# Kernel optimization log

Hardware: AMD Instinct MI355X
Metric: run time of the kernel (lower is better)

Reference implementation:

```python
import jax, jax.numpy as jnp
import numpy as np

LEAK = 0.2

def leaky(x):
    return jnp.where(x > 0, x, LEAK * x)

def relu(x):
    return jnp.maximum(x, 0)

def conv1d(x, w):
    # x [B,Cin,L], w [Cout,Cin,3], stride 1, padding 1
    return jax.lax.conv_general_dilated(x, w, (1,), [(1, 1)],
        dimension_numbers=('NCH', 'OIH', 'NCH'))

def conv2d(x, w, pad, dil=1, groups=1):
    return jax.lax.conv_general_dilated(x, w, (1, 1), [(pad, pad), (pad, pad)],
        rhs_dilation=(dil, dil), feature_group_count=groups,
        dimension_numbers=('NCHW', 'OIHW', 'NCHW'))

def bn2d(x, p, eps=1e-5):
    # p: [4,C] = gamma, beta, running_mean, running_var (eval-mode BN)
    g, b, m, v = p
    s = (1, -1, 1, 1)
    return (x - m.reshape(s)) * (g.reshape(s) / jnp.sqrt(v.reshape(s) + eps)) + b.reshape(s)

def layernorm(x, g, b, eps=1e-5):
    mu = x.mean(-1, keepdims=True)
    var = ((x - mu) ** 2).mean(-1, keepdims=True)
    return (x - mu) / jnp.sqrt(var + eps) * g + b

def l2n(x, axis, eps):
    n = jnp.sqrt((x * x).sum(axis, keepdims=True))
    return x / jnp.maximum(n, eps)


def setup_inputs() -> dict:
    key = jax.random.key(0)
    B, C, H, W = 4, 64, 48, 48
    D, Fn, T, V = 256, 8, 4, 16
    E = 16  # orthogonal prototype embed dim
    ks = iter(jax.random.split(key, 64))
    def rn(shape, s=0.05):
        return jax.random.normal(next(ks), shape, jnp.float32) * s
    def bnp(c):
        return jnp.stack([1.0 + rn((c,), 0.1), rn((c,), 0.1), rn((c,), 0.1), 1.0 + jnp.abs(rn((c,), 0.1))])
    return dict(
        basis_vector_bank=jax.random.normal(next(ks), (T, V, D), jnp.float32),
        task_f=jax.random.normal(next(ks), (B, C, 16, 16), jnp.float32),
        img_f=jax.random.normal(next(ks), (B, C, H, W), jnp.float32),
        protos=jax.random.normal(next(ks), (T, E), jnp.float32),
        tA_w1=rn((E // 4, 1, 3)), tA_w2=rn((E // 2, E // 4, 3)),
        iA_w=rn((E // 2, C, 3, 3)), iA_bn=bnp(E // 2),
        at_w1=rn((E, Fn // 2 * E)), at_b1=rn((Fn // 2 * E,)),
        at_ln_g=jnp.ones((Fn // 2 * E,)), at_ln_b=jnp.zeros((Fn // 2 * E,)),
        at_w2=rn((Fn // 2 * E, Fn * E)), at_b2=rn((Fn * E,)),
        bv_t1=rn((D // 4, 1, 3)), bv_t2=rn((D // 2, D // 4, 3)),
        bv_ic1=rn((D // 4, C, 3, 3)), bv_bn1=bnp(D // 4),
        bv_ic2=rn((D // 2, D // 4, 3, 3)), bv_bn2=bnp(D // 2),
        bv_w1=rn((D, D // 4)), bv_b1=rn((D // 4,)),
        bv_ln_g=jnp.ones((D // 4,)), bv_ln_b=jnp.zeros((D // 4,)),
        bv_w2=rn((D // 4, D)), bv_b2=rn((D,)),
        m1_w1=rn((D, D // 4)), m1_b1=rn((D // 4,)),
        m1_ln_g=jnp.ones((D // 4,)), m1_ln_b=jnp.zeros((D // 4,)),
        m1_w2=rn((D // 4, C * C)), m1_b2=rn((C * C,)),
        m3_w1=rn((D, D // 4)), m3_b1=rn((D // 4,)),
        m3_ln_g=jnp.ones((D // 4,)), m3_ln_b=jnp.zeros((D // 4,)),
        m3_w2=rn((D // 4, 9 * C * C)), m3_b2=rn((9 * C * C,)),
        blr_bn=bnp(C),
        zc_w=rn((C, C, 1, 1), 0.01), zc_b=rn((C,), 0.01),
    )


def _forward(basis_vector_bank, task_f, img_f, protos, tA_w1, tA_w2, iA_w, iA_bn,
             at_w1, at_b1, at_ln_g, at_ln_b, at_w2, at_b2,
             bv_t1, bv_t2, bv_ic1, bv_bn1, bv_ic2, bv_bn2,
             bv_w1, bv_b1, bv_ln_g, bv_ln_b, bv_w2, bv_b2,
             m1_w1, m1_b1, m1_ln_g, m1_ln_b, m1_w2, m1_b2,
             m3_w1, m3_b1, m3_ln_g, m3_ln_b, m3_w2, m3_b2,
             blr_bn, zc_w, zc_b):
    T, V, D = basis_vector_bank.shape
    B, C, H, W = img_f.shape
    E = protos.shape[1]
    Fn = at_w2.shape[1] // E
    tau = 0.5

    # --- A2SI routing features ---
    xt = task_f.reshape(B, 1, -1)
    t1 = conv1d(leaky(conv1d(xt, tA_w1)), tA_w2).mean(-1)          # [B,E/2]
    i1 = leaky(bn2d(conv2d(img_f, iA_w, 1), iA_bn)).mean((2, 3))   # [B,E/2]
    f1 = jnp.concatenate([t1, i1], axis=1)                         # [B,E]
    h = relu(layernorm(f1 @ at_w1 + at_b1, at_ln_g, at_ln_b))
    tif = (h @ at_w2 + at_b2).reshape(B, E, Fn)                    # [B,E,F]
    logits = jnp.einsum('te,bef->bft', l2n(protos, -1, 1e-8), l2n(tif, 1, 1e-8))  # [B,F,T]

    # hard gumbel-softmax (straight-through), fixed noise key for determinism
    u = jax.random.uniform(jax.random.key(42), logits.shape, jnp.float32, 1e-10, 1.0)
    g = -jnp.log(-jnp.log(u))
    y = jax.nn.softmax((logits + g) / tau, axis=-1)
    idx = jnp.argmax(y, axis=-1)                                   # [B,F]
    y_hard = jax.nn.one_hot(idx, T, dtype=y.dtype)
    set_type = y_hard + y - jax.lax.stop_gradient(y)

    bank_flat = basis_vector_bank.reshape(T, V * D)
    sbvb = jnp.einsum('bft,tk->bfk', set_type, bank_flat).reshape(B, Fn, V, D)

    # --- BasisV_filter: filter feature ---
    xt2 = task_f.reshape(B, C, -1)
    rms = jnp.sqrt((xt2 ** 2).mean((1, 2), keepdims=True))
    xt2 = (xt2 / (rms + 1e-8)).reshape(B, 1, -1)
    te = conv1d(leaky(conv1d(xt2, bv_t1)), bv_t2).mean(-1)         # [B,D/2]
    ie = leaky(bn2d(conv2d(img_f, bv_ic1, 1), bv_bn1))
    ie = leaky(bn2d(conv2d(ie, bv_ic2, 1), bv_bn2)).mean((2, 3))   # [B,D/2]
    ff = jnp.concatenate([te, ie], axis=1)                         # [B,D]
    ff = relu(layernorm(ff @ bv_w1 + bv_b1, bv_ln_g, bv_ln_b)) @ bv_w2 + bv_b2

    # --- per-(batch,type) group gather/top-k/scatter, vectorized ---
    # group bank = bank of first filter with that type (hard one-hot -> type's bank)
    occ = idx[:, None, :] == jnp.arange(T)[None, :, None]          # [B,T,F]
    first = jnp.argmax(occ, axis=-1)                               # [B,T]
    Bg = jnp.take_along_axis(sbvb, first[:, :, None, None], axis=1)  # [B,T,V,D]
    # all rows of Q within a group are identical (filter_f expanded over F),
    # so S.max(0) == cosine(ff[b], Bg[b,t])
    scores = jnp.einsum('bd,btvd->btv', l2n(ff, -1, 1e-12), l2n(Bg, -1, 1e-12))
    order = jnp.argsort(-scores, axis=-1)                          # [B,T,V] topk order
    lt = jnp.tril(jnp.ones((Fn, Fn), bool), -1)                    # j < i
    rank = ((idx[:, :, None] == idx[:, None, :]) & lt).sum(-1)     # position in group
    bidx = jnp.arange(B)[:, None]
    sel = order[bidx, idx, rank]                                   # [B,F]
    bvf = Bg[bidx, idx, sel]                                       # [B,F,D]

    # --- per-filter dynamic convolutions ---
    w1 = relu(layernorm(bvf @ m1_w1 + m1_b1, m1_ln_g, m1_ln_b)) @ m1_w2 + m1_b2
    w1 = w1.reshape(B, Fn, C, C)                                   # [B,F,out,in]
    w3 = relu(layernorm(bvf @ m3_w1 + m3_b1, m3_ln_g, m3_ln_b)) @ m3_w2 + m3_b2
    w3 = w3.reshape(B * Fn, C, C, 3, 3)

    dp0 = jnp.einsum('bfoc,bchw->bfohw', w1, img_f)                # 1x1 branch
    xin = jnp.broadcast_to(img_f[:, None], (B, Fn, C, H, W)).reshape(1, B * Fn * C, H, W)
    ker = w3.reshape(B * Fn * C, C, 3, 3)
    dpd = [conv2d(xin, ker, d, dil=d, groups=B * Fn).reshape(B, Fn, C, H, W)
           for d in (1, 2, 3)]                                     # same-padded dilated 3x3
    t_ = idx[:, :, None, None, None]
    dp = jnp.where(t_ == 0, dp0, jnp.where(t_ == 1, dpd[0],
         jnp.where(t_ == 2, dpd[1], dpd[2])))                      # [B,F,C,H,W]

    x = leaky(bn2d(dp.reshape(B * Fn, C, H, W), blr_bn)).reshape(B, Fn, C, H, W).mean(1)
    a = conv2d(x, zc_w, 0) + zc_b.reshape(1, -1, 1, 1)
    return a + img_f


@jax.jit
def reference(basis_vector_bank, task_f, img_f, protos, tA_w1, tA_w2, iA_w, iA_bn,
              at_w1, at_b1, at_ln_g, at_ln_b, at_w2, at_b2,
              bv_t1, bv_t2, bv_ic1, bv_bn1, bv_ic2, bv_bn2,
              bv_w1, bv_b1, bv_ln_g, bv_ln_b, bv_w2, bv_b2,
              m1_w1, m1_b1, m1_ln_g, m1_ln_b, m1_w2, m1_b2,
              m3_w1, m3_b1, m3_ln_g, m3_ln_b, m3_w2, m3_b2,
              blr_bn, zc_w, zc_b):
    return _forward(basis_vector_bank, task_f, img_f, protos, tA_w1, tA_w2, iA_w, iA_bn,
                    at_w1, at_b1, at_ln_g, at_ln_b, at_w2, at_b2,
                    bv_t1, bv_t2, bv_ic1, bv_bn1, bv_ic2, bv_bn2,
                    bv_w1, bv_b1, bv_ln_g, bv_ln_b, bv_w2, bv_b2,
                    m1_w1, m1_b1, m1_ln_g, m1_ln_b, m1_w2, m1_b2,
                    m3_w1, m3_b1, m3_ln_g, m3_ln_b, m3_w2, m3_b2,
                    blr_bn, zc_w, zc_b)
```

## Files before the change

kernel.cpp:

```cpp
#include <hip/hip_runtime.h>
#include <math.h>

#define LEAKC 0.2f

#define NB 4
#define NC 64
#define LLEN 16384
#define HW 2304
#define PP 54
#define PHW 2916
#define SLABP 72
#define CP 72
#define IE1C 50

typedef __attribute__((ext_vector_type(8))) short short8;
typedef __attribute__((ext_vector_type(4))) float floatx4;

__device__ __forceinline__ float leaky(float x){ return x > 0.f ? x : LEAKC*x; }

__device__ __forceinline__ float wave_sum64(float v){
  for(int off=32;off;off>>=1) v += __shfl_xor(v,off);
  return v;
}

__device__ __forceinline__ unsigned short f2bf(float x){
  unsigned u=__float_as_uint(x);
  unsigned r=u+0x7FFFu+((u>>16)&1u);
  return (unsigned short)(r>>16);
}

__device__ __forceinline__ void threefry2x32(unsigned k0, unsigned k1, unsigned& x0, unsigned& x1){
  unsigned ks0=k0, ks1=k1, ks2=k0^k1^0x1BD11BDAu;
  x0+=ks0; x1+=ks1;
  const int rot0[4]={13,15,26,6};
  const int rot1[4]={17,29,16,24};
#define TF_APPLY(rr) {for(int r=0;r<4;r++){x0+=x1; x1=(x1<<rr[r])|(x1>>(32-rr[r])); x1^=x0;}}
  TF_APPLY(rot0); x0+=ks1; x1+=ks2+1u;
  TF_APPLY(rot1); x0+=ks2; x1+=ks0+2u;
  TF_APPLY(rot0); x0+=ks0; x1+=ks1+3u;
  TF_APPLY(rot1); x0+=ks1; x1+=ks2+4u;
  TF_APPLY(rot0); x0+=ks2; x1+=ks0+5u;
#undef TF_APPLY
}

__device__ __forceinline__ float jax_uniform128(int i){
  unsigned x0=0u, x1=(unsigned)i;
  threefry2x32(0u,42u,x0,x1);
  unsigned bits = x0 ^ x1;
  unsigned fb=(bits>>9)|0x3f800000u;
  float f=__uint_as_float(fb)-1.0f;
  float u=f*(1.0f-1e-10f)+1e-10f;
  return fmaxf(1e-10f,u);
}

struct MidSM {
  float sT[64], s0[64], sL[64];
  float red8[64][9];
  float totA_s[4]; float rms_s;
  float part[512];
  float te_s[128], t1_s[8];
  float f1[16], h[64], tif[128], tifn[128], tden[8], pden[4], pn[64], z[32];
  int sidx[8], sfirst[4], srank[8], rows[8];
  float iered[128];
  float fbuf[256], hh[64], ffn_s[256], finv_s;
  float scores[64];
  int order[64];
  float bvf[2048];
};

__global__ __launch_bounds__(256) void k_pre(const float* __restrict__ task_f,
                      const float* __restrict__ w1A, const float* __restrict__ w1B,
                      float* __restrict__ totApart, float* __restrict__ a0A, float* __restrict__ aLA,
                      float* __restrict__ totBpart, float* __restrict__ a0B, float* __restrict__ aLB,
                      float* __restrict__ rmspart,
                      const float* __restrict__ img,
                      const float* __restrict__ w1, const float* __restrict__ w2,
                      const float* __restrict__ wa,
                      unsigned short* __restrict__ imgTP,
                      unsigned short* __restrict__ W1T, unsigned short* __restrict__ W2T,
                      unsigned short* __restrict__ WAT,
                      const float* __restrict__ mw1, const float* __restrict__ mw3,
                      const float* __restrict__ bvw1p, const float* __restrict__ bvw2p,
                      const float* __restrict__ bvt2p, const float* __restrict__ atw2p,
                      const float* __restrict__ bankp,
                      const float* __restrict__ m1w2p, const float* __restrict__ m3w2p,
                      const float* __restrict__ zcwp,
                      float* __restrict__ warm, int* __restrict__ donec){
  if(blockIdx.x<256){
    int b=blockIdx.x>>6, seg=blockIdx.x&63;
    const float* x=task_f+b*LLEN;
    float tA[4]={0,0,0,0};
    float tB[64];
#pragma unroll
    for(int c=0;c<64;c++) tB[c]=0.f;
    float sq=0.f;
    int l=seg*256+threadIdx.x;
    {
      float xm=(l>0)?x[l-1]:0.f;
      float xc=x[l];
      float xp=(l<LLEN-1)?x[l+1]:0.f;
      sq=xc*xc;
#pragma unroll
      for(int c=0;c<4;c++){
        float a=leaky(w1A[c*3+0]*xm + w1A[c*3+1]*xc + w1A[c*3+2]*xp);
        tA[c]=a;
        if(l==0) a0A[b*4+c]=a;
        if(l==LLEN-1) aLA[b*4+c]=a;
      }
#pragma unroll
      for(int c=0;c<64;c++){
        float a=leaky(w1B[c*3+0]*xm + w1B[c*3+1]*xc + w1B[c*3+2]*xp);
        tB[c]=a;
        if(l==0) a0B[b*64+c]=a;
        if(l==LLEN-1) aLB[b*64+c]=a;
      }
    }
    sq=wave_sum64(sq);
#pragma unroll
    for(int c=0;c<4;c++) tA[c]=wave_sum64(tA[c]);
#pragma unroll
    for(int c=0;c<64;c++){
      float v=tB[c];
      for(int off=32;off;off>>=1) v+=__shfl_down(v,off);
      tB[c]=v;
    }
    __shared__ float redB[4][64];
    __shared__ float redA[4][4];
    __shared__ float redQ[4];
    int wave=threadIdx.x>>6, lane=threadIdx.x&63;
    if(lane==0){
#pragma unroll
      for(int c=0;c<64;c++) redB[wave][c]=tB[c];
#pragma unroll
      for(int c=0;c<4;c++) redA[wave][c]=tA[c];
      redQ[wave]=sq;
    }
    __syncthreads();
    if(threadIdx.x<64){
      float s=redB[0][threadIdx.x]+redB[1][threadIdx.x]+redB[2][threadIdx.x]+redB[3][threadIdx.x];
      totBpart[(size_t)(b*64+seg)*64+threadIdx.x]=s;
    } else if(threadIdx.x<68){
      int c=threadIdx.x-64;
      totApart[(b*64+seg)*4+c]=redA[0][c]+redA[1][c]+redA[2][c]+redA[3][c];
    } else if(threadIdx.x==68){
      rmspart[b*64+seg]=redQ[0]+redQ[1]+redQ[2]+redQ[3];
    }
  } else if(blockIdx.x<400){
    int blk=blockIdx.x-256;
    int b=blk/36, t=blk%36;
    int p0=t*64;
    __shared__ float tile[64][65];
    int pp=threadIdx.x&63, c4=threadIdx.x>>6;
    for(int r=0;r<16;r++){
      int c=c4*16+r;
      tile[c][pp]=img[(b*64+c)*HW + p0+pp];
    }
    __syncthreads();
    int pxl=threadIdx.x>>2, cg=(threadIdx.x&3)*16;
    unsigned out[8];
#pragma unroll
    for(int q=0;q<8;q++){
      unsigned lo=f2bf(tile[cg+2*q][pxl]);
      unsigned hi=f2bf(tile[cg+2*q+1][pxl]);
      out[q]=lo|(hi<<16);
    }
    int px=p0+pxl;
    int h=px/48, w=px-h*48;
    int poff=(h+3)*PP+(w+3);
    unsigned* dst=(unsigned*)(imgTP + ((size_t)(b*PHW+poff))*64 + cg);
#pragma unroll
    for(int q=0;q<8;q++) dst[q]=out[q];
  } else if(blockIdx.x<868){
    int n=(blockIdx.x-400)*256+threadIdx.x;
    if(n<9*64*64){
      int tap=n>>12, oc=(n>>6)&63, c=n&63;
      W1T[n]=f2bf(w1[oc*576+c*9+tap]);
    } else if(n<9*64*64+9*128*64){
      int m=n-9*64*64;
      int tap=m/8192, r=m-tap*8192, oc=r>>6, c=r&63;
      W2T[m]=f2bf(w2[oc*576+c*9+tap]);
    } else {
      int q=n-9*64*64-9*128*64;
      if(q<9*16*64){
        int tap=q>>10, r=q&1023, o=r>>6, c=r&63;
        WAT[q]=(o<8)?f2bf(wa[o*576+c*9+tap]):(unsigned short)0;
      }
    }
  } else if(blockIdx.x<932){
    int t=(blockIdx.x-868)*256+threadIdx.x;
    float a=0.f;
    for(int i=t;i*16<16384;i+=16384) a+=mw1[i*16];
    for(int i=t;i*16<16384;i+=16384) a+=mw3[i*16];
    for(int i=t;i*16<16384;i+=16384) a+=bvw1p[i*16];
    for(int i=t;i*16<16384;i+=16384) a+=bvw2p[i*16];
    for(int i=t;i*16<24576;i+=16384) a+=bvt2p[i*16];
    for(int i=t;i*16<8192;i+=16384) a+=atw2p[i*16];
    for(int i=t;i*16<16384;i+=16384) a+=bankp[i*16];
    for(int i=t;i*16<262144;i+=16384) a+=m1w2p[i*16];
    for(int i=t;i*16<2359296;i+=16384) a+=m3w2p[i*16];
    for(int i=t;i*16<4096;i+=16384) a+=zcwp[i*16];
    warm[t&1023]=a;
  } else {
    if(blockIdx.x==932 && threadIdx.x==0) *donec=0;
    int id=(blockIdx.x-932)*256+threadIdx.x;
    uint4 z=make_uint4(0,0,0,0);
    for(int cch=id;cch<19584;cch+=4096){
      int ck=cch&7, pxid=cch>>3;
      int b=pxid/612, p=pxid-b*612;
      int h,w;
      if(p<324){ int r=p/54; w=p-r*54; h=(r<3)?r:(r+48); }
      else { int q=p-324; int r2=q/6; int cc=q-r2*6; h=3+r2; w=(cc<3)?cc:(cc+48); }
      *(uint4*)(imgTP + ((size_t)(b*PHW + h*PP + w))*64 + ck*8)=z;
    }
  }
}

__global__ __launch_bounds__(512) void k_cm(const unsigned short* __restrict__ imgTP,
    const unsigned short* __restrict__ W1T, const unsigned short* __restrict__ W2T,
    const unsigned short* __restrict__ WAT,
    const float* __restrict__ bn1, const float* __restrict__ bn2, const float* __restrict__ bnA,
    float* __restrict__ iepart, float* __restrict__ i1part,
    const float* __restrict__ totApart, const float* __restrict__ a0A, const float* __restrict__ aLA,
    const float* __restrict__ totBpart, const float* __restrict__ a0B, const float* __restrict__ aLB,
    const float* __restrict__ rmspart,
    const float* __restrict__ tA_w2, const float* __restrict__ bv_t2,
    const float* __restrict__ at_w1, const float* __restrict__ at_b1,
    const float* __restrict__ at_ln_g, const float* __restrict__ at_ln_b,
    const float* __restrict__ at_w2, const float* __restrict__ at_b2,
    const float* __restrict__ protos,
    const float* __restrict__ bv_w1, const float* __restrict__ bv_b1,
    const float* __restrict__ bv_ln_g, const float* __restrict__ bv_ln_b,
    const float* __restrict__ bv_w2, const float* __restrict__ bv_b2,
    const float* __restrict__ bank,
    const float* __restrict__ m1_w1, const float* __restrict__ m1_b1,
    const float* __restrict__ m1_g,  const float* __restrict__ m1_bb,
    const float* __restrict__ m3_w1, const float* __restrict__ m3_b1,
    const float* __restrict__ m3_g,  const float* __restrict__ m3_bb,
    int* __restrict__ idxo, float* __restrict__ hid1, float* __restrict__ hid3,
    int* __restrict__ donec){
  __shared__ __align__(16) char smraw[75456];
  int tid=threadIdx.x;
  int lane=tid&63, wv=tid>>6;
  int n0=lane&15, kg=lane>>4;
  if(blockIdx.x<96){
    int blk=blockIdx.x;
    int b=blk/24, hp=blk-b*24;
    int h0=hp*2;
    unsigned short* slab=(unsigned short*)smraw;
    unsigned short* ie1=(unsigned short*)(smraw+46656);
    {
      const unsigned short* ibase=imgTP+((size_t)b*PHW+(size_t)(h0+1)*PP)*64;
      for(int e=tid;e<6*54*8;e+=512){
        int rr=e/(54*8), rem=e-rr*54*8, w=rem>>3, ck=rem&7;
        uint4 v=*(const uint4*)(ibase+((size_t)(rr*PP+w))*64+ck*8);
        *(uint4*)(slab+(rr*54+w)*SLABP+ck*8)=v;
      }
      if(tid<64){
        int br=tid>>4, cq=(tid>>3)&1, ck=tid&7;
        *(uint4*)(ie1+((size_t)(br*IE1C+(cq?49:0)))*CP+ck*8)=make_uint4(0,0,0,0);
      }
    }
    __syncthreads();
    {
      int mt=wv&3, rh=wv>>2;
      floatx4 acc[2][3];
#pragma unroll
      for(int rr=0;rr<2;rr++)
#pragma unroll
        for(int nt=0;nt<3;nt++) acc[rr][nt]=(floatx4){0.f,0.f,0.f,0.f};
#pragma unroll
      for(int ti=0;ti<3;ti++){
#pragma unroll
        for(int tj=0;tj<3;tj++){
          int tap=ti*3+tj;
          const unsigned short* Ab=W1T+(size_t)tap*4096;
#pragma unroll
          for(int c0=0;c0<64;c0+=32){
            short8 a=*(const short8*)(Ab+((mt*16+n0)*64+c0+kg*8));
#pragma unroll
            for(int rr=0;rr<2;rr++){
              int sr=rh*2+rr+ti;
#pragma unroll
              for(int nt=0;nt<3;nt++){
                int sc=nt*16+n0+tj+2;
                short8 bv=*(const short8*)(slab+(sr*54+sc)*SLABP+c0+kg*8);
                acc[rr][nt]=__builtin_amdgcn_mfma_f32_16x16x32_bf16(a,bv,acc[rr][nt],0,0,0);
              }
            }
          }
        }
      }
      int obase=mt*16+kg*4;
      float scale[4],m_[4],be_[4];
#pragma unroll
      for(int reg=0;reg<4;reg++){
        int o=obase+reg;
        scale[reg]=bn1[o]/sqrtf(bn1[192+o]+1e-5f);
        m_[reg]=bn1[128+o]; be_[reg]=bn1[64+o];
      }
#pragma unroll
      for(int rr=0;rr<2;rr++){
        int br=rh*2+rr;
        bool rv=((unsigned)(h0-1+br))<48u;
#pragma unroll
        for(int nt=0;nt<3;nt++){
          float v0=rv?leaky((acc[rr][nt][0]-m_[0])*scale[0]+be_[0]):0.f;
          float v1=rv?leaky((acc[rr][nt][1]-m_[1])*scale[1]+be_[1]):0.f;
          float v2=rv?leaky((acc[rr][nt][2]-m_[2])*scale[2]+be_[2]):0.f;
          float v3=rv?leaky((acc[rr][nt][3]-m_[3])*scale[3]+be_[3]):0.f;
          unsigned w0=f2bf(v0)|((unsigned)f2bf(v1)<<16);
          unsigned w1=f2bf(v2)|((unsigned)f2bf(v3)<<16);
          uint2 pk={w0,w1};
          *(uint2*)(ie1+((size_t)(br*IE1C+(nt*16+1+n0)))*CP+obase)=pk;
        }
      }
    }
    __syncthreads();
    {
      int mt2=wv;
      floatx4 acc[6];
#pragma unroll
      for(int i=0;i<6;i++) acc[i]=(floatx4){0.f,0.f,0.f,0.f};
#pragma unroll
      for(int ti=0;ti<3;ti++){
#pragma unroll
        for(int tj=0;tj<3;tj++){
          int tap=ti*3+tj;
          const unsigned short* Ab=W2T+(size_t)tap*8192;
#pragma unroll
          for(int c0=0;c0<64;c0+=32){
            short8 a=*(const short8*)(Ab+((mt2*16+n0)*64+c0+kg*8));
#pragma unroll
            for(int rr=0;rr<2;rr++){
              int sr=rr+ti;
#pragma unroll
              for(int wc=0;wc<3;wc++){
                int q=wc*16+n0+tj;
                short8 bv=*(const short8*)(ie1+((size_t)(sr*IE1C+q))*CP+c0+kg*8);
                acc[rr*3+wc]=__builtin_amdgcn_mfma_f32_16x16x32_bf16(a,bv,acc[rr*3+wc],0,0,0);
              }
            }
          }
        }
      }
      int obase=mt2*16+kg*4;
#pragma unroll
      for(int reg=0;reg<4;reg++){
        int o=obase+reg;
        float scale=bn2[o]/sqrtf(bn2[384+o]+1e-5f);
        float m_=bn2[256+o], be_=bn2[128+o];
        float part=0;
#pragma unroll
        for(int i=0;i<6;i++) part+=leaky((acc[i][reg]-m_)*scale+be_);
        for(int off=1;off<16;off<<=1) part+=__shfl_xor(part,off);
        if(n0==0) iepart[(b*24+hp)*128+o]=part*(1.f/2304.f);
      }
    }
    __syncthreads();
    if(tid==0) __hip_atomic_fetch_add(donec,1,__ATOMIC_RELEASE,__HIP_MEMORY_SCOPE_AGENT);
  } else if(blockIdx.x<108){
    int blk2=blockIdx.x-96;
    int b=blk2/3, hg=blk2%3;
    int hp=hg*8+wv;
    int h0=hp*2;
    const unsigned short* ib=imgTP+(size_t)b*PHW*64;
    floatx4 acc[6];
#pragma unroll
    for(int i=0;i<6;i++) acc[i]=(floatx4){0.f,0.f,0.f,0.f};
#pragma unroll
    for(int ti=0;ti<3;ti++){
#pragma unroll
      for(int tj=0;tj<3;tj++){
        int tap=ti*3+tj;
        const unsigned short* Ab=WAT+(size_t)tap*1024;
#pragma unroll
        for(int c0=0;c0<64;c0+=32){
          short8 a=*(const short8*)(Ab+(n0*64+c0+kg*8));
#pragma unroll
          for(int rr=0;rr<2;rr++){
            int r=h0+rr+ti-1+3;
#pragma unroll
            for(int wc=0;wc<3;wc++){
              int w=wc*16+n0+tj-1+3;
              short8 bv=*(const short8*)(ib+((size_t)(r*PP+w)*64+c0+kg*8));
              acc[rr*3+wc]=__builtin_amdgcn_mfma_f32_16x16x32_bf16(a,bv,acc[rr*3+wc],0,0,0);
            }
          }
        }
      }
    }
    int obase=kg*4;
#pragma unroll
    for(int reg=0;reg<4;reg++){
      int o=obase+reg;
      float part=0;
      if(o<8){
        float scale=bnA[o]/sqrtf(bnA[24+o]+1e-5f);
        float m_=bnA[16+o], be_=bnA[8+o];
#pragma unroll
        for(int i=0;i<6;i++) part+=leaky((acc[i][reg]-m_)*scale+be_);
      }
      for(int off=1;off<16;off<<=1) part+=__shfl_xor(part,off);
      if(n0==0 && o<8) i1part[(b*24+hp)*8+o]=part*(1.f/2304.f);
    }
    __syncthreads();
    if(tid==0) __hip_atomic_fetch_add(donec,1,__ATOMIC_RELEASE,__HIP_MEMORY_SCOPE_AGENT);
  } else {
    MidSM* S=(MidSM*)smraw;
    int b=blockIdx.x-108;
    const float invL=1.0f/16384.0f;
    {
      int c8=tid>>3, g8=tid&7;
      float s8=0;
#pragma unroll
      for(int seg=g8*8;seg<g8*8+8;seg++) s8+=totBpart[(size_t)(b*64+seg)*64+c8];
      S->red8[c8][g8]=s8;
    }
    if(tid>=64 && tid<128){
      int t=tid-64;
      S->s0[t]=a0B[b*64+t]; S->sL[t]=aLB[b*64+t];
    } else if(tid>=128 && tid<192){
      float v=rmspart[b*64+(tid-128)];
      v=wave_sum64(v);
      if(tid==128) S->rms_s=v;
    } else if(tid>=192 && tid<196){
      int c=tid-192;
      float s=0;
#pragma unroll 8
      for(int seg=0;seg<64;seg++) s+=totApart[(b*64+seg)*4+c];
      S->totA_s[c]=s;
    }
    __syncthreads();
    if(tid<64){
      float s=0;
#pragma unroll
      for(int g=0;g<8;g++) s+=S->red8[tid][g];
      S->sT[tid]=s;
    }
    __syncthreads();
    float scB=1.0f/(sqrtf(S->rms_s*invL)+1e-8f);
    if(tid<256){
      int c2=tid&127, h2=tid>>7;
      const float* wr=bv_t2+c2*192;
      float s=0;
      for(int c1=h2*32;c1<h2*32+32;c1+=8){
        float4 q[6];
        const float4* r4=(const float4*)(wr+c1*3);
#pragma unroll
        for(int u=0;u<6;u++) q[u]=r4[u];
        const float* qq=(const float*)q;
#pragma unroll
        for(int u=0;u<8;u++){
          int c=c1+u;
          float T=S->sT[c], A0=S->s0[c], AL=S->sL[c];
          s += qq[u*3+0]*(T-AL) + qq[u*3+1]*T + qq[u*3+2]*(T-A0);
        }
      }
      S->part[tid]=s;
    } else if(tid>=384 && tid<392){
      int c2=tid-384;
      float s=0;
      for(int c1=0;c1<4;c1++){
        float T=S->totA_s[c1], A0=a0A[b*4+c1], AL=aLA[b*4+c1];
        const float* w=&tA_w2[(c2*4+c1)*3];
        s += w[0]*(T-AL) + w[1]*T + w[2]*(T-A0);
      }
      S->t1_s[c2]=s*invL;
    }
    __syncthreads();
    if(tid<128) S->te_s[tid]=(S->part[tid]+S->part[tid+128])*invL*scB;
    __syncthreads();
    if(tid==0){
      while(__hip_atomic_load(donec,__ATOMIC_ACQUIRE,__HIP_MEMORY_SCOPE_AGENT)<108)
        __builtin_amdgcn_s_sleep(8);
    }
    __syncthreads();
    if(tid<8) S->f1[tid]=S->t1_s[tid];
    else if(tid<16){
      int f=tid-8;
      float s=0;
#pragma unroll
      for(int g=0;g<24;g++) s+=i1part[(b*24+g)*8+f];
      S->f1[tid]=s;
    } else if(tid>=256 && tid<384){
      int c=tid-256;
      float s=0;
#pragma unroll 8
      for(int g=0;g<24;g++) s+=iepart[(b*24+g)*128+c];
      S->iered[c]=s;
    }
    __syncthreads();
    if(tid<64){
      float s=at_b1[lane];
#pragma unroll
      for(int i=0;i<16;i++) s+=S->f1[i]*at_w1[i*64+lane];
      float mu=wave_sum64(s)*(1.f/64.f);
      float d=s-mu;
      float var=wave_sum64(d*d)*(1.f/64.f);
      S->h[lane]=fmaxf(d*(1.0f/sqrtf(var+1e-5f))*at_ln_g[lane]+at_ln_b[lane],0.f);
    }
    __syncthreads();
    if(tid<256){
      int n=tid&127, h2=tid>>7;
      float a0=0,a1=0;
      for(int k=h2*32;k<h2*32+32;k+=2){
        a0+=S->h[k]*at_w2[k*128+n];
        a1+=S->h[k+1]*at_w2[(k+1)*128+n];
      }
      S->part[tid]=a0+a1;
    }
    __syncthreads();
    if(tid<128) S->tif[tid]=at_b2[tid]+S->part[tid]+S->part[tid+128];
    __syncthreads();
    if(tid<8){
      int f=tid;
      float ss=0; for(int e=0;e<16;e++){float v=S->tif[e*8+f]; ss+=v*v;}
      S->tden[f]=fmaxf(sqrtf(ss),1e-8f);
    } else if(tid<12){
      int t=tid-8;
      float ss=0; for(int e=0;e<16;e++){float v=protos[t*16+e]; ss+=v*v;}
      S->pden[t]=fmaxf(sqrtf(ss),1e-8f);
    }
    __syncthreads();
    if(tid<128) S->tifn[tid]=S->tif[tid]/S->tden[tid&7];
    if(tid<64) S->pn[tid]=protos[tid]/S->pden[tid>>4];
    __syncthreads();
    if(tid<32){
      int f=tid>>2, t=tid&3;
      float ss=0;
#pragma unroll
      for(int e=0;e<16;e++) ss+=S->pn[t*16+e]*S->tifn[e*8+f];
      float u=jax_uniform128(b*32+f*4+t);
      float g=-logf(-logf(u));
      S->z[tid]=ss+g;
    }
    __syncthreads();
    if(tid<8){
      float best=S->z[tid*4]; int bi=0;
      for(int t=1;t<4;t++){ float v=S->z[tid*4+t]; if(v>best){best=v;bi=t;} }
      S->sidx[tid]=bi;
    }
    __syncthreads();
    if(tid<4){
      int t=tid;
      int fi=0;
      for(int f=7;f>=0;f--) if(S->sidx[f]==t) fi=f;
      S->sfirst[t]=fi;
    } else if(tid<12){
      int f=tid-4;
      int c=0; for(int f2=0;f2<f;f2++) if(S->sidx[f2]==S->sidx[f]) c++;
      S->srank[f]=c;
    }
    __syncthreads();

    if(tid<128) S->fbuf[tid]=S->te_s[tid];
    else if(tid<256) S->fbuf[tid]=S->iered[tid-128];
    __syncthreads();
    if(tid<256){
      int l64=tid&63, q=tid>>6;
      float a0=0,a1=0,a2=0,a3=0;
      for(int k=q*64;k<q*64+64;k+=4){
        a0+=S->fbuf[k]  *bv_w1[k*64+l64];
        a1+=S->fbuf[k+1]*bv_w1[(k+1)*64+l64];
        a2+=S->fbuf[k+2]*bv_w1[(k+2)*64+l64];
        a3+=S->fbuf[k+3]*bv_w1[(k+3)*64+l64];
      }
      S->part[tid]=((a0+a1)+(a2+a3));
    }
    __syncthreads();
    if(tid<64){
      float s=bv_b1[lane]+S->part[lane]+S->part[64+lane]+S->part[128+lane]+S->part[192+lane];
      float mu=wave_sum64(s)*(1.f/64.f);
      float d=s-mu;
      float var=wave_sum64(d*d)*(1.f/64.f);
      S->hh[lane]=fmaxf(d*(1.0f/sqrtf(var+1e-5f))*bv_ln_g[lane]+bv_ln_b[lane],0.f);
    }
    __syncthreads();
    {
      int n=tid&255, h2=tid>>8;
      float a0=0,a1=0;
      for(int k=h2*32;k<h2*32+32;k+=2){
        a0+=S->hh[k]*bv_w2[k*256+n];
        a1+=S->hh[k+1]*bv_w2[(k+1)*256+n];
      }
      S->part[tid]=a0+a1;
    }
    __syncthreads();
    if(tid<256) S->ffn_s[tid]=bv_b2[tid]+S->part[tid]+S->part[tid+256];
    __syncthreads();
    if(tid<64){
      float sq=0;
#pragma unroll
      for(int u=0;u<4;u++){ float v=S->ffn_s[u*64+lane]; sq+=v*v; }
      sq=wave_sum64(sq);
      if(lane==0) S->finv_s=1.0f/fmaxf(sqrtf(sq),1e-12f);
    }
    __syncthreads();
    if(tid<256) S->ffn_s[tid]*=S->finv_s;
    __syncthreads();

    if(tid<128){
      int it=tid&63, h2=tid>>6;
      int t=it>>4, v=it&15;
      int tt=S->sidx[S->sfirst[t]];
      const float4* row=(const float4*)(bank+(tt*16+v)*256);
      float sa=0,na=0;
      for(int d4=h2*32;d4<h2*32+32;d4++){
        float4 r=row[d4];
        const float* fp=&S->ffn_s[d4*4];
        sa+=fp[0]*r.x+fp[1]*r.y+fp[2]*r.z+fp[3]*r.w;
        na+=r.x*r.x+r.y*r.y+r.z*r.z+r.w*r.w;
      }
      S->part[tid]=sa;
      S->part[256+tid]=na;
    }
    __syncthreads();
    if(tid<64) S->scores[tid]=(S->part[tid]+S->part[tid+64])/fmaxf(sqrtf(S->part[256+tid]+S->part[320+tid]),1e-12f);
    __syncthreads();
    if(tid<4){
      const float* sc=&S->scores[tid*16];
      unsigned used=0;
      for(int pk=0;pk<16;pk++){
        int best=-1; float bv=-1e30f;
        for(int v2=0;v2<16;v2++){
          if(used&(1u<<v2)) continue;
          float vv=sc[v2];
          if(best<0||vv>bv){bv=vv;best=v2;}
        }
        used|=1u<<best;
        S->order[tid*16+pk]=best;
      }
    }
    __syncthreads();
    if(tid<8){
      int t=S->sidx[tid];
      int v=S->order[t*16+S->srank[tid]];
      S->rows[tid]=t*16+v;
      idxo[b*8+tid]=t;
    }
    __syncthreads();

    for(int ii=tid;ii<2048;ii+=512){
      int r=ii>>8, d=ii&255;
      S->bvf[ii]=bank[S->rows[r]*256+d];
    }
    __syncthreads();
    {
      int r=wv;
      const float* bp=&S->bvf[r*256];
      float a0=0,a1=0,a2=0,a3=0;
      float c0=0,c1=0,c2=0,c3=0;
      for(int d=0;d<256;d+=4){
        float b0=bp[d],b1=bp[d+1],b2=bp[d+2],b3=bp[d+3];
        a0+=b0*m1_w1[d*64+lane];
        a1+=b1*m1_w1[(d+1)*64+lane];
        a2+=b2*m1_w1[(d+2)*64+lane];
        a3+=b3*m1_w1[(d+3)*64+lane];
        c0+=b0*m3_w1[d*64+lane];
        c1+=b1*m3_w1[(d+1)*64+lane];
        c2+=b2*m3_w1[(d+2)*64+lane];
        c3+=b3*m3_w1[(d+3)*64+lane];
      }
      float s1=m1_b1[lane]+((a0+a1)+(a2+a3));
      float s3=m3_b1[lane]+((c0+c1)+(c2+c3));
      float mu=wave_sum64(s1)*(1.f/64.f);
      float dd=s1-mu;
      float var=wave_sum64(dd*dd)*(1.f/64.f);
      hid1[(b*8+r)*64+lane]=fmaxf(dd*(1.0f/sqrtf(var+1e-5f))*m1_g[lane]+m1_bb[lane],0.f);
      mu=wave_sum64(s3)*(1.f/64.f);
      dd=s3-mu;
      var=wave_sum64(dd*dd)*(1.f/64.f);
      hid3[(b*8+r)*64+lane]=fmaxf(dd*(1.0f/sqrtf(var+1e-5f))*m3_g[lane]+m3_bb[lane],0.f);
    }
  }
}

__global__ __launch_bounds__(256) void k_heads(const float* __restrict__ hid1, const float* __restrict__ hid3,
                        const float* __restrict__ w2a, const float* __restrict__ b2a,
                        const float* __restrict__ w2b, const float* __restrict__ b2b,
                        unsigned short* __restrict__ A1, unsigned short* __restrict__ A3){
  __shared__ float hl[2048];
  if(blockIdx.x<16){
    int n=blockIdx.x*256+threadIdx.x;
    float wcol[64];
#pragma unroll
    for(int k=0;k<64;k++) wcol[k]=w2a[k*4096+n];
    float bb=b2a[n];
    for(int i=threadIdx.x;i<2048;i+=256) hl[i]=hid1[i];
    __syncthreads();
    for(int bf=0;bf<32;bf++){
      float s=bb;
#pragma unroll
      for(int k=0;k<64;k++) s+=hl[bf*64+k]*wcol[k];
      A1[bf*4096+n]=f2bf(s);
    }
  } else {
    int n=(blockIdx.x-16)*256+threadIdx.x;
    float wcol[64];
#pragma unroll
    for(int k=0;k<64;k++) wcol[k]=w2b[(size_t)k*36864+n];
    float bb=b2b[n];
    for(int i=threadIdx.x;i<2048;i+=256) hl[i]=hid3[i];
    __syncthreads();
    int o=n/576, rem=n-o*576;
    int c=rem/9, tap=rem-c*9;
    size_t base=((size_t)tap*64+o)*64+c;
    for(int bf=0;bf<32;bf++){
      float s=bb;
#pragma unroll
      for(int k=0;k<64;k++) s+=hl[bf*64+k]*wcol[k];
      A3[(size_t)bf*9*4096+base]=f2bf(s);
    }
  }
}

__global__ __launch_bounds__(512) void k_dynF(const unsigned short* __restrict__ imgTP,
                       const unsigned short* __restrict__ A1, const unsigned short* __restrict__ A3,
                       const int* __restrict__ idx, const float* __restrict__ bn,
                       const float* __restrict__ zc_w, const float* __restrict__ zc_b,
                       const float* __restrict__ img, float* __restrict__ out){
  int blk=blockIdx.x;
  int b=blk/48, r0=blk-b*48;
  int tid=threadIdx.x;
  int lane=tid&63, w8=tid>>6;
  int mt=w8&3, fh=w8>>2;
  int n0=lane&15, kg=lane>>4;
  __shared__ unsigned short slab[7*54*SLABP];
  __shared__ float xl[64*50];
  __shared__ float zl[4096];
  int tts[4];
#pragma unroll
  for(int i=0;i<4;i++) tts[i]=idx[b*8+fh*4+i];
  int obase=mt*16+kg*4;
  float scale[4],m_[4],be_[4];
#pragma unroll
  for(int reg=0;reg<4;reg++){
    int o=obase+reg;
    scale[reg]=bn[o]/sqrtf(bn[192+o]+1e-5f);
    m_[reg]=bn[128+o]; be_[reg]=bn[64+o];
  }
  for(int i=tid;i<4096;i+=512) zl[i]=zc_w[i];
  for(int i=tid;i<3200;i+=512) xl[i]=0.f;
  {
    const unsigned short* ibase=imgTP+((size_t)b*PHW+(size_t)r0*PP)*64;
    for(int e=tid;e<7*54*8;e+=512){
      int rr=e/(54*8), rem=e-rr*54*8, w=rem>>3, ck=rem&7;
      uint4 v=*(const uint4*)(ibase + ((size_t)(rr*PP+w))*64 + ck*8);
      *(uint4*)(slab + (rr*54+w)*SLABP + ck*8)=v;
    }
  }
  __syncthreads();
  float xsum[3][4];
#pragma unroll
  for(int wc=0;wc<3;wc++)
#pragma unroll
    for(int reg=0;reg<4;reg++) xsum[wc][reg]=0.f;
#pragma unroll
  for(int fi=0;fi<4;fi++){
    int f=fh*4+fi;
    int bf=b*8+f;
    int tt=tts[fi];
    floatx4 acc[3];
#pragma unroll
    for(int i=0;i<3;i++) acc[i]=(floatx4){0.f,0.f,0.f,0.f};
    if(tt==0){
      const unsigned short* Ab=A1+(size_t)bf*4096;
#pragma unroll
      for(int c0=0;c0<64;c0+=32){
        short8 a=*(const short8*)(Ab+((mt*16+n0)*64+c0+kg*8));
#pragma unroll
        for(int wc=0;wc<3;wc++){
          short8 bv=*(const short8*)(slab + (3*54 + wc*16+n0+3)*SLABP + c0+kg*8);
          acc[wc]=__builtin_amdgcn_mfma_f32_16x16x32_bf16(a,bv,acc[wc],0,0,0);
        }
      }
    } else {
      int d=tt;
      const unsigned short* A3b=A3+(size_t)bf*9*4096;
#pragma unroll
      for(int ti=0;ti<3;ti++){
        int lr=d*(ti-1)+3;
#pragma unroll
        for(int tj=0;tj<3;tj++){
          int tap=ti*3+tj;
          int dw=d*(tj-1)+3;
          const unsigned short* Ab=A3b+(size_t)tap*4096;
#pragma unroll
          for(int c0=0;c0<64;c0+=32){
            short8 a=*(const short8*)(Ab+((mt*16+n0)*64+c0+kg*8));
#pragma unroll
            for(int wc=0;wc<3;wc++){
              short8 bv=*(const short8*)(slab + (lr*54 + wc*16+n0+dw)*SLABP + c0+kg*8);
              acc[wc]=__builtin_amdgcn_mfma_f32_16x16x32_bf16(a,bv,acc[wc],0,0,0);
            }
          }
        }
      }
    }
#pragma unroll
    for(int wc=0;wc<3;wc++)
#pragma unroll
      for(int reg=0;reg<4;reg++)
        xsum[wc][reg]+=leaky((acc[wc][reg]-m_[reg])*scale[reg]+be_[reg]);
  }
#pragma unroll
  for(int wc=0;wc<3;wc++)
#pragma unroll
    for(int reg=0;reg<4;reg++)
      atomicAdd(&xl[(obase+reg)*50 + wc*16+n0], xsum[wc][reg]*0.125f);
  __syncthreads();
  size_t base=(size_t)b*64*HW + r0*48;
  for(int e=tid;e<3072;e+=512){
    int o=e/48, px=e-o*48;
    float s=zc_b[o];
#pragma unroll
    for(int c=0;c<64;c++) s+=zl[o*64+c]*xl[c*50+px];
    size_t a=base+(size_t)o*HW+px;
    out[a]=s+img[a];
  }
}

extern "C" void kernel_launch(void* const* d_in, const int* in_sizes, int n_in,
                              void* d_out, int out_size, void* d_ws, size_t ws_size,
                              hipStream_t stream){
  const float* bank   =(const float*)d_in[0];
  const float* task_f =(const float*)d_in[1];
  const float* img_f  =(const float*)d_in[2];
  const float* protos =(const float*)d_in[3];
  const float* tA_w1  =(const float*)d_in[4];
  const float* tA_w2  =(const float*)d_in[5];
  const float* iA_w   =(const float*)d_in[6];
  const float* iA_bn  =(const float*)d_in[7];
  const float* at_w1  =(const float*)d_in[8];
  const float* at_b1  =(const float*)d_in[9];
  const float* at_ln_g=(const float*)d_in[10];
  const float* at_ln_b=(const float*)d_in[11];
  const float* at_w2  =(const float*)d_in[12];
  const float* at_b2  =(const float*)d_in[13];
  const float* bv_t1  =(const float*)d_in[14];
  const float* bv_t2  =(const float*)d_in[15];
  const float* bv_ic1 =(const float*)d_in[16];
  const float* bv_bn1 =(const float*)d_in[17];
  const float* bv_ic2 =(const float*)d_in[18];
  const float* bv_bn2 =(const float*)d_in[19];
  const float* bv_w1  =(const float*)d_in[20];
  const float* bv_b1  =(const float*)d_in[21];
  const float* bv_ln_g=(const float*)d_in[22];
  const float* bv_ln_b=(const float*)d_in[23];
  const float* bv_w2  =(const float*)d_in[24];
  const float* bv_b2  =(const float*)d_in[25];
  const float* m1_w1  =(const float*)d_in[26];
  const float* m1_b1  =(const float*)d_in[27];
  const float* m1_ln_g=(const float*)d_in[28];
  const float* m1_ln_b=(const float*)d_in[29];
  const float* m1_w2  =(const float*)d_in[30];
  const float* m1_b2  =(const float*)d_in[31];
  const float* m3_w1  =(const float*)d_in[32];
  const float* m3_b1  =(const float*)d_in[33];
  const float* m3_ln_g=(const float*)d_in[34];
  const float* m3_ln_b=(const float*)d_in[35];
  const float* m3_w2  =(const float*)d_in[36];
  const float* m3_b2  =(const float*)d_in[37];
  const float* blr_bn =(const float*)d_in[38];
  const float* zc_w   =(const float*)d_in[39];
  const float* zc_b   =(const float*)d_in[40];

  float* ws=(float*)d_ws;
  float* totApart=ws+0;
  float* a0A  =ws+1024;
  float* aLA  =ws+1040;
  float* totBpart=ws+1056;
  float* a0B  =ws+17440;
  float* aLB  =ws+17696;
  float* rmspart=ws+17952;
  float* i1part =ws+18208;
  float* iepart =ws+18976;
  int*   idxp   =(int*)(ws+31264);
  float* hid1=ws+31296;
  float* hid3=ws+33344;
  unsigned short* A1p  =(unsigned short*)(ws+35392);
  unsigned short* A3p  =(unsigned short*)(ws+100928);
  unsigned short* imgTP=(unsigned short*)(ws+690752);
  unsigned short* W1Tp =(unsigned short*)(ws+1064000);
  unsigned short* W2Tp =(unsigned short*)(ws+1082432);
  unsigned short* WATp =(unsigned short*)(ws+1119296);
  float* warm =ws+1123904;
  int*   donec=(int*)(ws+1124928);

  k_pre<<<948,256,0,stream>>>(task_f, tA_w1, bv_t1,
                              totApart, a0A, aLA, totBpart, a0B, aLB, rmspart,
                              img_f, bv_ic1, bv_ic2, iA_w, imgTP, W1Tp, W2Tp, WATp,
                              m1_w1, m3_w1, bv_w1, bv_w2, bv_t2, at_w2, bank,
                              m1_w2, m3_w2, zc_w, warm, donec);
  k_cm<<<112,512,0,stream>>>(imgTP, W1Tp, W2Tp, WATp, bv_bn1, bv_bn2, iA_bn,
                             iepart, i1part,
                             totApart, a0A, aLA, totBpart, a0B, aLB, rmspart,
                             tA_w2, bv_t2,
                             at_w1, at_b1, at_ln_g, at_ln_b, at_w2, at_b2, protos,
                             bv_w1, bv_b1, bv_ln_g, bv_ln_b, bv_w2, bv_b2, bank,
                             m1_w1, m1_b1, m1_ln_g, m1_ln_b,
                             m3_w1, m3_b1, m3_ln_g, m3_ln_b,
                             idxp, hid1, hid3, donec);
  k_heads<<<160,256,0,stream>>>(hid1, hid3, m1_w2, m1_b2, m3_w2, m3_b2, A1p, A3p);
  k_dynF<<<192,512,0,stream>>>(imgTP, A1p, A3p, idxp, blr_bn, zc_w, zc_b, img_f, (float*)d_out);

  (void)in_sizes; (void)n_in; (void)out_size; (void)ws_size;
}
```

Measured before the change: 266.1 us.

## Fuse head GEMV kernel into k_cm with per-stage atomic counters

Removes the separate k_heads launch by adding 80 extra blocks to k_cm that prefetch their weight columns into registers and then spin-wait on a counter set by the four mid blocks before computing A1/A3. The single done counter is split into per-stage counters, so the mid blocks wait only on the 12 i1 blocks first and defer the wait on the 96 conv blocks until the iepart reduction is actually needed. This overlaps weight loading and mid-stage work with the conv blocks and removes one launch boundary. The cost is extra spinning blocks, and correctness depends on all 192 blocks being co-resident to avoid deadlock.

```diff
diff --git a/kernel.cpp b/kernel.cpp
--- a/kernel.cpp
+++ b/kernel.cpp
@@ -61,7 +61,6 @@
   float te_s[128], t1_s[8];
   float f1[16], h[64], tif[128], tifn[128], tden[8], pden[4], pn[64], z[32];
   int sidx[8], sfirst[4], srank[8], rows[8];
-  float iered[128];
   float fbuf[256], hh[64], ffn_s[256], finv_s;
   float scores[64];
   int order[64];
@@ -85,7 +84,7 @@
                       const float* __restrict__ bankp,
                       const float* __restrict__ m1w2p, const float* __restrict__ m3w2p,
                       const float* __restrict__ zcwp,
-                      float* __restrict__ warm, int* __restrict__ donec){
+                      float* __restrict__ warm, int* __restrict__ cnt){
   if(blockIdx.x<256){
     int b=blockIdx.x>>6, seg=blockIdx.x&63;
     const float* x=task_f+b*LLEN;
@@ -201,7 +200,8 @@
     for(int i=t;i*16<4096;i+=16384) a+=zcwp[i*16];
     warm[t&1023]=a;
   } else {
-    if(blockIdx.x==932 && threadIdx.x==0) *donec=0;
+    if(blockIdx.x==932 && threadIdx.x<4)
+      __hip_atomic_store(&cnt[threadIdx.x],0,__ATOMIC_RELAXED,__HIP_MEMORY_SCOPE_AGENT);
     int id=(blockIdx.x-932)*256+threadIdx.x;
     uint4 z=make_uint4(0,0,0,0);
     for(int cch=id;cch<19584;cch+=4096){
@@ -236,8 +236,11 @@
     const float* __restrict__ m1_g,  const float* __restrict__ m1_bb,
     const float* __restrict__ m3_w1, const float* __restrict__ m3_b1,
     const float* __restrict__ m3_g,  const float* __restrict__ m3_bb,
+    const float* __restrict__ m1_w2, const float* __restrict__ m1_b2,
+    const float* __restrict__ m3_w2, const float* __restrict__ m3_b2,
+    unsigned short* __restrict__ A1, unsigned short* __restrict__ A3,
     int* __restrict__ idxo, float* __restrict__ hid1, float* __restrict__ hid3,
-    int* __restrict__ donec){
+    int* __restrict__ cnt){
   __shared__ __align__(16) char smraw[75456];
   int tid=threadIdx.x;
   int lane=tid&63, wv=tid>>6;
@@ -357,7 +360,7 @@
       }
     }
     __syncthreads();
-    if(tid==0) __hip_atomic_fetch_add(donec,1,__ATOMIC_RELEASE,__HIP_MEMORY_SCOPE_AGENT);
+    if(tid==0) __hip_atomic_fetch_add(&cnt[0],1,__ATOMIC_RELEASE,__HIP_MEMORY_SCOPE_AGENT);
   } else if(blockIdx.x<108){
     int blk2=blockIdx.x-96;
     int b=blk2/3, hg=blk2%3;
@@ -404,8 +407,8 @@
       if(n0==0 && o<8) i1part[(b*24+hp)*8+o]=part*(1.f/2304.f);
     }
     __syncthreads();
-    if(tid==0) __hip_atomic_fetch_add(donec,1,__ATOMIC_RELEASE,__HIP_MEMORY_SCOPE_AGENT);
-  } else {
+    if(tid==0) __hip_atomic_fetch_add(&cnt[1],1,__ATOMIC_RELEASE,__HIP_MEMORY_SCOPE_AGENT);
+  } else if(blockIdx.x<112){
     MidSM* S=(MidSM*)smraw;
     int b=blockIdx.x-108;
     const float invL=1.0f/16384.0f;
@@ -471,7 +474,7 @@
     if(tid<128) S->te_s[tid]=(S->part[tid]+S->part[tid+128])*invL*scB;
     __syncthreads();
     if(tid==0){
-      while(__hip_atomic_load(donec,__ATOMIC_ACQUIRE,__HIP_MEMORY_SCOPE_AGENT)<108)
+      while(__hip_atomic_load(&cnt[1],__ATOMIC_ACQUIRE,__HIP_MEMORY_SCOPE_AGENT)<12)
         __builtin_amdgcn_s_sleep(8);
     }
     __syncthreads();
@@ -482,12 +485,6 @@
 #pragma unroll
       for(int g=0;g<24;g++) s+=i1part[(b*24+g)*8+f];
       S->f1[tid]=s;
-    } else if(tid>=256 && tid<384){
-      int c=tid-256;
-      float s=0;
-#pragma unroll 8
-      for(int g=0;g<24;g++) s+=iepart[(b*24+g)*128+c];
-      S->iered[c]=s;
     }
     __syncthreads();
     if(tid<64){
@@ -552,9 +549,19 @@
       S->srank[f]=c;
     }
     __syncthreads();
-
+    if(tid==0){
+      while(__hip_atomic_load(&cnt[0],__ATOMIC_ACQUIRE,__HIP_MEMORY_SCOPE_AGENT)<96)
+        __builtin_amdgcn_s_sleep(8);
+    }
+    __syncthreads();
     if(tid<128) S->fbuf[tid]=S->te_s[tid];
-    else if(tid<256) S->fbuf[tid]=S->iered[tid-128];
+    else if(tid<256){
+      int c=tid-128;
+      float s=0;
+#pragma unroll 8
+      for(int g=0;g<24;g++) s+=iepart[(b*24+g)*128+c];
+      S->fbuf[tid]=s;
+    }
     __syncthreads();
     if(tid<256){
       int l64=tid&63, q=tid>>6;
@@ -672,44 +679,52 @@
       var=wave_sum64(dd*dd)*(1.f/64.f);
       hid3[(b*8+r)*64+lane]=fmaxf(dd*(1.0f/sqrtf(var+1e-5f))*m3_g[lane]+m3_bb[lane],0.f);
     }
-  }
-}
-
-__global__ __launch_bounds__(256) void k_heads(const float* __restrict__ hid1, const float* __restrict__ hid3,
-                        const float* __restrict__ w2a, const float* __restrict__ b2a,
-                        const float* __restrict__ w2b, const float* __restrict__ b2b,
-                        unsigned short* __restrict__ A1, unsigned short* __restrict__ A3){
-  __shared__ float hl[2048];
-  if(blockIdx.x<16){
-    int n=blockIdx.x*256+threadIdx.x;
-    float wcol[64];
-#pragma unroll
-    for(int k=0;k<64;k++) wcol[k]=w2a[k*4096+n];
-    float bb=b2a[n];
-    for(int i=threadIdx.x;i<2048;i+=256) hl[i]=hid1[i];
-    __syncthreads();
-    for(int bf=0;bf<32;bf++){
-      float s=bb;
-#pragma unroll
-      for(int k=0;k<64;k++) s+=hl[bf*64+k]*wcol[k];
-      A1[bf*4096+n]=f2bf(s);
-    }
+    __syncthreads();
+    if(tid==0) __hip_atomic_fetch_add(&cnt[2],1,__ATOMIC_RELEASE,__HIP_MEMORY_SCOPE_AGENT);
   } else {
-    int n=(blockIdx.x-16)*256+threadIdx.x;
-    float wcol[64];
-#pragma unroll
-    for(int k=0;k<64;k++) wcol[k]=w2b[(size_t)k*36864+n];
-    float bb=b2b[n];
-    for(int i=threadIdx.x;i<2048;i+=256) hl[i]=hid3[i];
-    __syncthreads();
-    int o=n/576, rem=n-o*576;
-    int c=rem/9, tap=rem-c*9;
-    size_t base=((size_t)tap*64+o)*64+c;
-    for(int bf=0;bf<32;bf++){
-      float s=bb;
-#pragma unroll
-      for(int k=0;k<64;k++) s+=hl[bf*64+k]*wcol[k];
-      A3[(size_t)bf*9*4096+base]=f2bf(s);
+    int hblk=blockIdx.x-112;
+    float* hl=(float*)smraw;
+    if(hblk<8){
+      int n=hblk*512+tid;
+      float wcol[64];
+#pragma unroll
+      for(int k=0;k<64;k++) wcol[k]=m1_w2[k*4096+n];
+      float bb=m1_b2[n];
+      if(tid==0){
+        while(__hip_atomic_load(&cnt[2],__ATOMIC_ACQUIRE,__HIP_MEMORY_SCOPE_AGENT)<4)
+          __builtin_amdgcn_s_sleep(8);
+      }
+      __syncthreads();
+      for(int i=tid;i<2048;i+=512) hl[i]=hid1[i];
+      __syncthreads();
+      for(int bf=0;bf<32;bf++){
+        float s=bb;
+#pragma unroll
+        for(int k=0;k<64;k++) s+=hl[bf*64+k]*wcol[k];
+        A1[bf*4096+n]=f2bf(s);
+      }
+    } else {
+      int n=(hblk-8)*512+tid;
+      float wcol[64];
+#pragma unroll
+      for(int k=0;k<64;k++) wcol[k]=m3_w2[(size_t)k*36864+n];
+      float bb=m3_b2[n];
+      if(tid==0){
+        while(__hip_atomic_load(&cnt[2],__ATOMIC_ACQUIRE,__HIP_MEMORY_SCOPE_AGENT)<4)
+          __builtin_amdgcn_s_sleep(8);
+      }
+      __syncthreads();
+      for(int i=tid;i<2048;i+=512) hl[i]=hid3[i];
+      __syncthreads();
+      int o=n/576, rem=n-o*576;
+      int c=rem/9, tap=rem-c*9;
+      size_t base=((size_t)tap*64+o)*64+c;
+      for(int bf=0;bf<32;bf++){
+        float s=bb;
+#pragma unroll
+        for(int k=0;k<64;k++) s+=hl[bf*64+k]*wcol[k];
+        A3[(size_t)bf*9*4096+base]=f2bf(s);
+      }
     }
   }
 }
@@ -885,14 +900,14 @@
   unsigned short* W2Tp =(unsigned short*)(ws+1082432);
   unsigned short* WATp =(unsigned short*)(ws+1119296);
   float* warm =ws+1123904;
-  int*   donec=(int*)(ws+1124928);
+  int*   cnt  =(int*)(ws+1124928);
 
   k_pre<<<948,256,0,stream>>>(task_f, tA_w1, bv_t1,
                               totApart, a0A, aLA, totBpart, a0B, aLB, rmspart,
                               img_f, bv_ic1, bv_ic2, iA_w, imgTP, W1Tp, W2Tp, WATp,
                               m1_w1, m3_w1, bv_w1, bv_w2, bv_t2, at_w2, bank,
-                              m1_w2, m3_w2, zc_w, warm, donec);
-  k_cm<<<112,512,0,stream>>>(imgTP, W1Tp, W2Tp, WATp, bv_bn1, bv_bn2, iA_bn,
+                              m1_w2, m3_w2, zc_w, warm, cnt);
+  k_cm<<<192,512,0,stream>>>(imgTP, W1Tp, W2Tp, WATp, bv_bn1, bv_bn2, iA_bn,
                              iepart, i1part,
                              totApart, a0A, aLA, totBpart, a0B, aLB, rmspart,
                              tA_w2, bv_t2,
@@ -900,8 +915,9 @@
                              bv_w1, bv_b1, bv_ln_g, bv_ln_b, bv_w2, bv_b2, bank,
                              m1_w1, m1_b1, m1_ln_g, m1_ln_b,
                              m3_w1, m3_b1, m3_ln_g, m3_ln_b,
-                             idxp, hid1, hid3, donec);
-  k_heads<<<160,256,0,stream>>>(hid1, hid3, m1_w2, m1_b2, m3_w2, m3_b2, A1p, A3p);
+                             m1_w2, m1_b2, m3_w2, m3_b2,
+                             A1p, A3p,
+                             idxp, hid1, hid3, cnt);
   k_dynF<<<192,512,0,stream>>>(imgTP, A1p, A3p, idxp, blr_bn, zc_w, zc_b, img_f, (float*)d_out);
 
   (void)in_sizes; (void)n_in; (void)out_size; (void)ws_size;
```

Result: slower. 283.0 us (+6.3%).
